# Performance work log

Hardware: AMD Instinct MI355X
Metric: run time of the kernel (lower is better)

Reference implementation:

```python
import math
import jax, jax.numpy as jnp
from jax import lax
import numpy as np

L, B, S, D, H, F = 12, 8, 512, 768, 12, 3072
DH = D // H
REL_POS_BINS, MAX_REL_POS = 32, 128
REL_2D_POS_BINS, MAX_REL_2D_POS = 64, 256
LN_EPS = 1e-12


def _rel_bucket(rel, num_buckets, max_distance):
    # bidirectional relative_position_bucket as in LayoutLMv2
    num_buckets = num_buckets // 2
    ret = (rel > 0).astype(jnp.int32) * num_buckets
    n = jnp.abs(rel)
    max_exact = num_buckets // 2
    is_small = n < max_exact
    n_safe = jnp.maximum(n, 1)  # avoid log(0); masked by is_small anyway
    val_if_large = max_exact + (
        jnp.log(n_safe.astype(jnp.float32) / max_exact)
        / math.log(max_distance / max_exact) * (num_buckets - max_exact)
    ).astype(jnp.int32)
    val_if_large = jnp.minimum(val_if_large, num_buckets - 1)
    return ret + jnp.where(is_small, n.astype(jnp.int32), val_if_large)


def _layernorm(x, g, b):
    mu = jnp.mean(x, axis=-1, keepdims=True)
    var = jnp.var(x, axis=-1, keepdims=True)
    return (x - mu) * lax.rsqrt(var + LN_EPS) * g + b


def _encoder(hidden_states, attention_mask, position_ids, bbox,
             qkv_w, q_bias, v_bias, attn_out_w, attn_out_b, ln1_g, ln1_b,
             inter_w, inter_b, ffn_out_w, ffn_out_b, ln2_g, ln2_b,
             rel_pos_table, rel_x_table, rel_y_table):
    b, s, d = hidden_states.shape
    h = rel_pos_table.shape[1]
    dh = d // h
    # 1D relative position bias: [B,H,S,S]
    rel = position_ids[:, None, :] - position_ids[:, :, None]  # [B,S,S], rel[b,i,j]=p[j]-p[i]
    rp = _rel_bucket(rel, REL_POS_BINS, MAX_REL_POS)
    bias = jnp.transpose(rel_pos_table[rp], (0, 3, 1, 2))
    # 2D spatial bias from bbox x (coord 0) and y (coord 3)
    cx = bbox[:, :, 0]
    cy = bbox[:, :, 3]
    bx = _rel_bucket(cx[:, None, :] - cx[:, :, None], REL_2D_POS_BINS, MAX_REL_2D_POS)
    by = _rel_bucket(cy[:, None, :] - cy[:, :, None], REL_2D_POS_BINS, MAX_REL_2D_POS)
    bias = bias + jnp.transpose(rel_x_table[bx] + rel_y_table[by], (0, 3, 1, 2))
    mask = attention_mask.astype(bool)  # [B,1,1,S], True = masked
    inv_sqrt_dh = 1.0 / math.sqrt(dh)

    def layer(carry, p):
        (qw, qb, vb, aow, aob, g1, b1, iw, ib, fow, fob, g2, b2) = p
        qkv = carry @ qw                      # [B,S,3D] (fast_qkv, no bias)
        q, k, v = jnp.split(qkv, 3, axis=-1)
        q = (q + qb) * inv_sqrt_dh
        v = v + vb
        q = q.reshape(b, s, h, dh)
        k = k.reshape(b, s, h, dh)
        v = v.reshape(b, s, h, dh)
        scores = jnp.einsum('bihd,bjhd->bhij', q, k) + bias
        scores = jnp.where(mask, -jnp.inf, scores.astype(jnp.float32))
        probs = jax.nn.softmax(scores, axis=-1).astype(carry.dtype)
        ctx = jnp.einsum('bhij,bjhd->bihd', probs, v).reshape(b, s, d)
        attn = _layernorm(ctx @ aow + aob + carry, g1, b1)
        ff = jax.nn.gelu(attn @ iw + ib, approximate=False)
        out = _layernorm(ff @ fow + fob + attn, g2, b2)
        return out, None

    params = (qkv_w, q_bias, v_bias, attn_out_w, attn_out_b, ln1_g, ln1_b,
              inter_w, inter_b, ffn_out_w, ffn_out_b, ln2_g, ln2_b)
    out, _ = lax.scan(layer, hidden_states, params)
    return out


def setup_inputs() -> dict:
    key = jax.random.key(0)
    ks = jax.random.split(key, 12)
    w = 0.02
    inp = {
        'hidden_states': jax.random.normal(ks[0], (B, S, D), jnp.float32),
        'attention_mask': jax.random.randint(ks[1], (B, 1, 1, S), 0, 2).astype(jnp.int32),
        'position_ids': jnp.broadcast_to(jnp.arange(S, dtype=jnp.int64), (B, S)),
        'bbox': jax.random.randint(ks[2], (B, S, 4), 0, 1000).astype(jnp.int64),
        'qkv_w': jax.random.normal(ks[3], (L, D, 3 * D), jnp.float32) * w,
        'q_bias': jnp.zeros((L, D), jnp.float32),
        'v_bias': jnp.zeros((L, D), jnp.float32),
        'attn_out_w': jax.random.normal(ks[4], (L, D, D), jnp.float32) * w,
        'attn_out_b': jnp.zeros((L, D), jnp.float32),
        'ln1_g': jnp.ones((L, D), jnp.float32),
        'ln1_b': jnp.zeros((L, D), jnp.float32),
        'inter_w': jax.random.normal(ks[5], (L, D, F), jnp.float32) * w,
        'inter_b': jnp.zeros((L, F), jnp.float32),
        'ffn_out_w': jax.random.normal(ks[6], (L, F, D), jnp.float32) * w,
        'ffn_out_b': jnp.zeros((L, D), jnp.float32),
        'ln2_g': jnp.ones((L, D), jnp.float32),
        'ln2_b': jnp.zeros((L, D), jnp.float32),
        'rel_pos_table': jax.random.normal(ks[7], (REL_POS_BINS, H), jnp.float32) * w,
        'rel_x_table': jax.random.normal(ks[8], (REL_2D_POS_BINS, H), jnp.float32) * w,
        'rel_y_table': jax.random.normal(ks[9], (REL_2D_POS_BINS, H), jnp.float32) * w,
    }
    return inp


def reference(hidden_states, attention_mask, position_ids, bbox,
              qkv_w, q_bias, v_bias, attn_out_w, attn_out_b, ln1_g, ln1_b,
              inter_w, inter_b, ffn_out_w, ffn_out_b, ln2_g, ln2_b,
              rel_pos_table, rel_x_table, rel_y_table):
    return _encoder(hidden_states, attention_mask, position_ids, bbox,
                    qkv_w, q_bias, v_bias, attn_out_w, attn_out_b, ln1_g, ln1_b,
                    inter_w, inter_b, ffn_out_w, ffn_out_b, ln2_g, ln2_b,
                    rel_pos_table, rel_x_table, rel_y_table)
```

## Files before the change

### kernel.cpp

```cpp
#include <hip/hip_runtime.h>
#include <hip/hip_bf16.h>
#include <cstdint>

#define LCONST 12
#define BCONST 8
#define SCONST 512
#define DCONST 768
#define HCONST 12
#define FCONST 3072
#define DH 64

typedef __bf16 bf16x8 __attribute__((ext_vector_type(8)));
typedef float f32x4 __attribute__((ext_vector_type(4)));

__device__ __forceinline__ void gload16(const void* g, void* l) {
    __builtin_amdgcn_global_load_lds(
            (const __attribute__((address_space(1))) void*)g,
            (__attribute__((address_space(3))) void*)l, 16, 0, 0);
}

__device__ __forceinline__ int rbucket(int rel, int nb2, int maxex) {
    int ret = (rel > 0) ? nb2 : 0;
    int n = (rel < 0) ? -rel : rel;
    if (n < maxex) return ret + n;
    const float inv_ln16 = 0.36067376022224085f;
    int v = maxex + (int)(logf((float)n / (float)maxex) * inv_ln16 * (float)(nb2 - maxex));
    if (v > nb2 - 1) v = nb2 - 1;
    return ret + v;
}

__global__ __launch_bounds__(256) void build_idx_kernel(
        const int* __restrict__ pos, const int* __restrict__ bbox,
        int* __restrict__ idx) {
    size_t t = (size_t)blockIdx.x * 256 + threadIdx.x;
    int j = (int)(t & 511);
    int i = (int)((t >> 9) & 511);
    int b = (int)(t >> 18);
    int rp = rbucket(pos[b * SCONST + j] - pos[b * SCONST + i], 16, 8);
    int cxi = bbox[((size_t)b * SCONST + i) * 4 + 0];
    int cxj = bbox[((size_t)b * SCONST + j) * 4 + 0];
    int cyi = bbox[((size_t)b * SCONST + i) * 4 + 3];
    int cyj = bbox[((size_t)b * SCONST + j) * 4 + 3];
    int bx = rbucket(cxj - cxi, 32, 16);
    int by = rbucket(cyj - cyi, 32, 16);
    idx[t] = rp | (bx << 5) | (by << 11);
}

__global__ __launch_bounds__(256) void cvt_kernel(const float* __restrict__ in,
                                                  __bf16* __restrict__ out, int n) {
    int t = blockIdx.x * 256 + threadIdx.x;
    if (t < n) out[t] = (__bf16)in[t];
}

__global__ __launch_bounds__(256) void transpose_cvt_kernel(
        const float* __restrict__ in, __bf16* __restrict__ out, int R, int C) {
    __shared__ float tile[32][33];
    size_t off = (size_t)blockIdx.y * R * C;
    int nct = C >> 5;
    int c0 = (blockIdx.x % nct) << 5;
    int r0 = (blockIdx.x / nct) << 5;
    int tx = threadIdx.x & 31, ty = threadIdx.x >> 5;
#pragma unroll
    for (int i = 0; i < 32; i += 8)
        tile[ty + i][tx] = in[off + (size_t)(r0 + ty + i) * C + c0 + tx];
    __syncthreads();
#pragma unroll
    for (int i = 0; i < 32; i += 8)
        out[off + (size_t)(c0 + ty + i) * R + r0 + tx] = (__bf16)tile[tx][ty + i];
}

template <int MODE>
__global__ __launch_bounds__(256) void gemm_kernel(
        const __bf16* __restrict__ A, const __bf16* __restrict__ Bt,
        int M, int N, int Kc, int ldK,
        const float* __restrict__ cbias, const float* __restrict__ vbias,
        float* __restrict__ part,
        __bf16* __restrict__ outQ, __bf16* __restrict__ outK,
        __bf16* __restrict__ outV, __bf16* __restrict__ outB) {
    __shared__ __align__(16) __bf16 As[128 * 32];
    __shared__ __align__(16) __bf16 Bs[128 * 32];
    int tid = threadIdx.x;
    int wid = tid >> 6, lane = tid & 63, quad = lane >> 4, l16 = lane & 15;
    int nTM = M >> 7;
    int tileM = (blockIdx.x % nTM) << 7;
    int tileN = (blockIdx.x / nTM) << 7;
    int chunk = blockIdx.y;
    int wm = wid >> 1, wn = wid & 1;

    const __bf16* Ab = A + (size_t)chunk * Kc;
    const __bf16* Bb = Bt + (size_t)chunk * Kc;
    const __bf16* gA0 = Ab + (size_t)(tileM + wid * 32 + (lane >> 2)) * ldK + ((lane & 3) << 3);
    const __bf16* gB0 = Bb + (size_t)(tileN + wid * 32 + (lane >> 2)) * ldK + ((lane & 3) << 3);
    __bf16* lA0 = As + wid * 1024;
    __bf16* lB0 = Bs + wid * 1024;

    f32x4 acc[4][4] = {};

    for (int k0 = 0; k0 < Kc; k0 += 32) {
        gload16(gA0 + k0, lA0);
        gload16(gA0 + (size_t)16 * ldK + k0, lA0 + 512);
        gload16(gB0 + k0, lB0);
        gload16(gB0 + (size_t)16 * ldK + k0, lB0 + 512);
        __syncthreads();
        bf16x8 af[4], bfr[4];
#pragma unroll
        for (int mt = 0; mt < 4; mt++)
            af[mt] = *(const bf16x8*)&As[(wm * 64 + mt * 16 + l16) * 32 + quad * 8];
#pragma unroll
        for (int nt = 0; nt < 4; nt++)
            bfr[nt] = *(const bf16x8*)&Bs[(wn * 64 + nt * 16 + l16) * 32 + quad * 8];
#pragma unroll
        for (int mt = 0; mt < 4; mt++)
#pragma unroll
            for (int nt = 0; nt < 4; nt++)
                acc[mt][nt] = __builtin_amdgcn_mfma_f32_16x16x32_bf16(
                        af[mt], bfr[nt], acc[mt][nt], 0, 0, 0);
        __syncthreads();
    }

#pragma unroll
    for (int mt = 0; mt < 4; mt++)
#pragma unroll
        for (int nt = 0; nt < 4; nt++)
#pragma unroll
            for (int r = 0; r < 4; r++) {
                int row = tileM + wm * 64 + mt * 16 + quad * 4 + r;
                int col = tileN + wn * 64 + nt * 16 + l16;
                float v = acc[mt][nt][r];
                if (MODE == 0) {
                    int b = row >> 9, s = row & 511;
                    if (col < 768) {
                        int h = col >> 6, dh = col & 63;
                        float q = (v + cbias[col]) * 0.125f;
                        outQ[(((size_t)b * HCONST + h) * SCONST + s) * DH + dh] = (__bf16)q;
                    } else if (col < 1536) {
                        int c2 = col - 768;
                        int h = c2 >> 6, dh = c2 & 63;
                        outK[(((size_t)b * HCONST + h) * SCONST + s) * DH + dh] = (__bf16)v;
                    } else {
                        int c2 = col - 1536;
                        int h = c2 >> 6, dh = c2 & 63;
                        float vv = v + vbias[c2];
                        outV[(((size_t)b * HCONST + h) * DH + dh) * SCONST + s] = (__bf16)vv;
                    }
                } else if (MODE == 2) {
                    float u = v + cbias[col];
                    float g = 0.5f * u * (1.0f + erff(u * 0.70710678118654752f));
                    outB[(size_t)row * N + col] = (__bf16)g;
                } else {
                    part[(size_t)chunk * M * N + (size_t)row * N + col] = v;
                }
            }
}

__global__ __launch_bounds__(256) void attn_kernel(
        const __bf16* __restrict__ qbuf, const __bf16* __restrict__ kbuf,
        const __bf16* __restrict__ vbuf, const int* __restrict__ idx,
        const int* __restrict__ amask, const float* __restrict__ tpg,
        const float* __restrict__ txg, const float* __restrict__ tyg,
        __bf16* __restrict__ ctx) {
    int bh = blockIdx.x >> 3;
    int i0 = (blockIdx.x & 7) << 6;
    int b = bh / HCONST, h = bh % HCONST;

    __shared__ __align__(16) __bf16 Ks[64 * 64];
    __shared__ __align__(16) __bf16 Vs[64 * 64];
    __shared__ __align__(16) __bf16 Ps[4][16 * 64];
    __shared__ float tp[32], tx[64], ty[64];
    __shared__ float mk[512];

    int tid = threadIdx.x;
    if (tid < 32) tp[tid] = tpg[tid * HCONST + h];
    if (tid < 64) {
        tx[tid] = txg[tid * HCONST + h];
        ty[tid] = tyg[tid * HCONST + h];
    }
    for (int j = tid; j < 512; j += 256)
        mk[j] = amask[b * SCONST + j] ? -INFINITY : 0.0f;

    int wid = tid >> 6, lane = tid & 63, quad = lane >> 4, l16 = lane & 15;

    const __bf16* qrow = qbuf + ((size_t)bh * SCONST + i0 + wid * 16 + l16) * DH;
    bf16x8 qf0 = *(const bf16x8*)(qrow + quad * 8);
    bf16x8 qf1 = *(const bf16x8*)(qrow + 32 + quad * 8);

    const __bf16* kg = kbuf + (size_t)bh * SCONST * DH;
    const __bf16* vg = vbuf + (size_t)bh * DH * SCONST;

    f32x4 O[4] = {};
    float m_r[4] = {-1e30f, -1e30f, -1e30f, -1e30f};
    float l_r[4] = {0.f, 0.f, 0.f, 0.f};

    __syncthreads();

    for (int j0 = 0; j0 < SCONST; j0 += 64) {
        {
            const __bf16* kbase = kg + (size_t)j0 * DH;
#pragma unroll
            for (int s = 0; s < 2; s++) {
                int c = wid * 2 + s;
                gload16(kbase + c * 512 + lane * 8, Ks + c * 512);
                int dh = c * 8 + (lane >> 3), cc = lane & 7;
                gload16(vg + (size_t)dh * SCONST + j0 + cc * 8, Vs + c * 512);
            }
        }
        __syncthreads();

        float sc[4][4];
#pragma unroll
        for (int jt = 0; jt < 4; jt++) {
            f32x4 a = {};
            bf16x8 kf0 = *(const bf16x8*)&Ks[(jt * 16 + l16) * 64 + quad * 8];
            bf16x8 kf1 = *(const bf16x8*)&Ks[(jt * 16 + l16) * 64 + 32 + quad * 8];
            a = __builtin_amdgcn_mfma_f32_16x16x32_bf16(qf0, kf0, a, 0, 0, 0);
            a = __builtin_amdgcn_mfma_f32_16x16x32_bf16(qf1, kf1, a, 0, 0, 0);
#pragma unroll
            for (int r = 0; r < 4; r++) {
                int i = i0 + wid * 16 + quad * 4 + r;
                int j = j0 + jt * 16 + l16;
                int pk = idx[((size_t)b * SCONST + i) * SCONST + j];
                float bias = tp[pk & 31] + tx[(pk >> 5) & 63] + ty[(pk >> 11) & 63];
                sc[jt][r] = a[r] + bias + mk[j];
            }
        }

        float p[4][4];
#pragma unroll
        for (int r = 0; r < 4; r++) {
            float mb = fmaxf(fmaxf(sc[0][r], sc[1][r]), fmaxf(sc[2][r], sc[3][r]));
#pragma unroll
            for (int m = 1; m < 16; m <<= 1) mb = fmaxf(mb, __shfl_xor(mb, m, 64));
            float mn = fmaxf(m_r[r], mb);
            float alpha = __expf(m_r[r] - mn);
            m_r[r] = mn;
            float ls = 0.f;
#pragma unroll
            for (int jt = 0; jt < 4; jt++) {
                float pv = __expf(sc[jt][r] - mn);
                p[jt][r] = pv;
                ls += pv;
            }
#pragma unroll
            for (int m = 1; m < 16; m <<= 1) ls += __shfl_xor(ls, m, 64);
            l_r[r] = l_r[r] * alpha + ls;
#pragma unroll
            for (int nt = 0; nt < 4; nt++) O[nt][r] *= alpha;
        }

        __bf16* pl = &Ps[wid][0];
#pragma unroll
        for (int jt = 0; jt < 4; jt++)
#pragma unroll
            for (int r = 0; r < 4; r++)
                pl[(quad * 4 + r) * 64 + jt * 16 + l16] = (__bf16)p[jt][r];

        bf16x8 pa0 = *(const bf16x8*)&pl[l16 * 64 + quad * 8];
        bf16x8 pa1 = *(const bf16x8*)&pl[l16 * 64 + 32 + quad * 8];
#pragma unroll
        for (int nt = 0; nt < 4; nt++) {
            bf16x8 vb0 = *(const bf16x8*)&Vs[(nt * 16 + l16) * 64 + quad * 8];
            bf16x8 vb1 = *(const bf16x8*)&Vs[(nt * 16 + l16) * 64 + 32 + quad * 8];
            O[nt] = __builtin_amdgcn_mfma_f32_16x16x32_bf16(pa0, vb0, O[nt], 0, 0, 0);
            O[nt] = __builtin_amdgcn_mfma_f32_16x16x32_bf16(pa1, vb1, O[nt], 0, 0, 0);
        }
        __syncthreads();
    }

#pragma unroll
    for (int nt = 0; nt < 4; nt++)
#pragma unroll
        for (int r = 0; r < 4; r++) {
            int i = i0 + wid * 16 + quad * 4 + r;
            int dh = nt * 16 + l16;
            float o = O[nt][r] / l_r[r];
            ctx[((size_t)b * SCONST + i) * DCONST + h * DH + dh] = (__bf16)o;
        }
}

__global__ __launch_bounds__(256) void ln4_kernel(
        const float* __restrict__ part, const float* __restrict__ resid,
        const float* __restrict__ cbias, const float* __restrict__ g,
        const float* __restrict__ bb, float* __restrict__ outF,
        __bf16* __restrict__ outB) {
    const size_t MN = (size_t)4096 * DCONST;
    __shared__ float red[4];
    int row = blockIdx.x, t = threadIdx.x;
    size_t o = (size_t)row * DCONST;
    float v0, v1, v2;
    {
        int c0 = t, c1 = t + 256, c2 = t + 512;
        v0 = part[o + c0] + part[MN + o + c0] + part[2 * MN + o + c0] +
             part[3 * MN + o + c0] + cbias[c0] + resid[o + c0];
        v1 = part[o + c1] + part[MN + o + c1] + part[2 * MN + o + c1] +
             part[3 * MN + o + c1] + cbias[c1] + resid[o + c1];
        v2 = part[o + c2] + part[MN + o + c2] + part[2 * MN + o + c2] +
             part[3 * MN + o + c2] + cbias[c2] + resid[o + c2];
    }
    float s = v0 + v1 + v2;
#pragma unroll
    for (int m = 1; m < 64; m <<= 1) s += __shfl_xor(s, m, 64);
    if ((t & 63) == 0) red[t >> 6] = s;
    __syncthreads();
    s = red[0] + red[1] + red[2] + red[3];
    __syncthreads();
    float mu = s * (1.0f / 768.0f);
    float d0 = v0 - mu, d1 = v1 - mu, d2 = v2 - mu;
    float q = d0 * d0 + d1 * d1 + d2 * d2;
#pragma unroll
    for (int m = 1; m < 64; m <<= 1) q += __shfl_xor(q, m, 64);
    if ((t & 63) == 0) red[t >> 6] = q;
    __syncthreads();
    q = red[0] + red[1] + red[2] + red[3];
    float rstd = rsqrtf(q * (1.0f / 768.0f) + 1e-12f);
    float y0 = d0 * rstd * g[t] + bb[t];
    float y1 = d1 * rstd * g[t + 256] + bb[t + 256];
    float y2 = d2 * rstd * g[t + 512] + bb[t + 512];
    outF[o + t] = y0;
    outF[o + t + 256] = y1;
    outF[o + t + 512] = y2;
    outB[o + t] = (__bf16)y0;
    outB[o + t + 256] = (__bf16)y1;
    outB[o + t + 512] = (__bf16)y2;
}

extern "C" void kernel_launch(void* const* d_in, const int* in_sizes, int n_in,
                              void* d_out, int out_size, void* d_ws, size_t ws_size,
                              hipStream_t stream) {
    const float* hidden = (const float*)d_in[0];
    const int* amask = (const int*)d_in[1];
    const int* pos = (const int*)d_in[2];
    const int* bbox = (const int*)d_in[3];
    const float* qkv_w = (const float*)d_in[4];
    const float* q_bias = (const float*)d_in[5];
    const float* v_bias = (const float*)d_in[6];
    const float* aow = (const float*)d_in[7];
    const float* aob = (const float*)d_in[8];
    const float* ln1g = (const float*)d_in[9];
    const float* ln1b = (const float*)d_in[10];
    const float* iw = (const float*)d_in[11];
    const float* ib = (const float*)d_in[12];
    const float* fow = (const float*)d_in[13];
    const float* fob = (const float*)d_in[14];
    const float* ln2g = (const float*)d_in[15];
    const float* ln2b = (const float*)d_in[16];
    const float* tpt = (const float*)d_in[17];
    const float* txt = (const float*)d_in[18];
    const float* tyt = (const float*)d_in[19];
    float* out = (float*)d_out;

    char* w = (char*)d_ws;
    size_t used = 0;
    auto carve = [&](size_t bytes) {
        char* p = w + used;
        used += (bytes + 255) & ~(size_t)255;
        return p;
    };
    const size_t MT = 4096;
    __bf16* qbuf = (__bf16*)carve(MT * 768 * 2);
    __bf16* kbuf = (__bf16*)carve(MT * 768 * 2);
    __bf16* vbuf = (__bf16*)carve(MT * 768 * 2);
    __bf16* xbf = (__bf16*)carve(MT * 768 * 2);
    __bf16* ctxbf = (__bf16*)carve(MT * 768 * 2);
    float* attnf = (float*)carve(MT * 768 * 4);
    __bf16* attnbf = (__bf16*)carve(MT * 768 * 2);
    __bf16* ffbf = (__bf16*)carve(MT * 3072 * 2);
    float* part = (float*)carve(4 * MT * 768 * 4);
    int* idxb = (int*)carve((size_t)BCONST * SCONST * SCONST * 4);

    const size_t wq_sz = (size_t)2304 * 768 * 2;
    const size_t wa_sz = (size_t)768 * 768 * 2;
    const size_t wi_sz = (size_t)3072 * 768 * 2;
    const size_t wf_sz = (size_t)768 * 3072 * 2;
    const size_t wsum = wq_sz + wa_sz + wi_sz + wf_sz;
    bool full = (ws_size >= used + 12 * wsum + (12 * 4 + 4) * 256);
    int nlw = full ? 12 : 1;
    __bf16* wqT = (__bf16*)carve(wq_sz * nlw);
    __bf16* waT = (__bf16*)carve(wa_sz * nlw);
    __bf16* wiT = (__bf16*)carve(wi_sz * nlw);
    __bf16* wfT = (__bf16*)carve(wf_sz * nlw);

    build_idx_kernel<<<(BCONST * SCONST * SCONST) / 256, 256, 0, stream>>>(pos, bbox, idxb);
    cvt_kernel<<<(int)(MT * 768 / 256), 256, 0, stream>>>(hidden, xbf, (int)(MT * 768));

    if (full) {
        transpose_cvt_kernel<<<dim3((2304 / 32) * (768 / 32), 12), 256, 0, stream>>>(
                qkv_w, wqT, 768, 2304);
        transpose_cvt_kernel<<<dim3((768 / 32) * (768 / 32), 12), 256, 0, stream>>>(
                aow, waT, 768, 768);
        transpose_cvt_kernel<<<dim3((3072 / 32) * (768 / 32), 12), 256, 0, stream>>>(
                iw, wiT, 768, 3072);
        transpose_cvt_kernel<<<dim3((768 / 32) * (3072 / 32), 12), 256, 0, stream>>>(
                fow, wfT, 3072, 768);
    }

    for (int l = 0; l < LCONST; l++) {
        __bf16* wq_l = wqT + (full ? (size_t)l * 2304 * 768 : 0);
        __bf16* wa_l = waT + (full ? (size_t)l * 768 * 768 : 0);
        __bf16* wi_l = wiT + (full ? (size_t)l * 3072 * 768 : 0);
        __bf16* wf_l = wfT + (full ? (size_t)l * 768 * 3072 : 0);
        if (!full) {
            transpose_cvt_kernel<<<dim3((2304 / 32) * (768 / 32), 1), 256, 0, stream>>>(
                    qkv_w + (size_t)l * 768 * 2304, wq_l, 768, 2304);
            transpose_cvt_kernel<<<dim3((768 / 32) * (768 / 32), 1), 256, 0, stream>>>(
                    aow + (size_t)l * 768 * 768, wa_l, 768, 768);
            transpose_cvt_kernel<<<dim3((3072 / 32) * (768 / 32), 1), 256, 0, stream>>>(
                    iw + (size_t)l * 768 * 3072, wi_l, 768, 3072);
            transpose_cvt_kernel<<<dim3((768 / 32) * (3072 / 32), 1), 256, 0, stream>>>(
                    fow + (size_t)l * 3072 * 768, wf_l, 3072, 768);
        }

        gemm_kernel<0><<<dim3((4096 / 128) * (2304 / 128), 1), 256, 0, stream>>>(
                xbf, wq_l, 4096, 2304, 768, 768, q_bias + (size_t)l * 768,
                v_bias + (size_t)l * 768, nullptr, qbuf, kbuf, vbuf, nullptr);

        attn_kernel<<<BCONST * HCONST * (SCONST / 64), 256, 0, stream>>>(
                qbuf, kbuf, vbuf, idxb, amask, tpt, txt, tyt, ctxbf);

        gemm_kernel<4><<<dim3((4096 / 128) * (768 / 128), 4), 256, 0, stream>>>(
                ctxbf, wa_l, 4096, 768, 192, 768, nullptr, nullptr, part,
                nullptr, nullptr, nullptr, nullptr);
        const float* xres = (l == 0) ? hidden : out;
        ln4_kernel<<<4096, 256, 0, stream>>>(part, xres, aob + (size_t)l * 768,
                                             ln1g + (size_t)l * 768,
                                             ln1b + (size_t)l * 768, attnf, attnbf);

        gemm_kernel<2><<<dim3((4096 / 128) * (3072 / 128), 1), 256, 0, stream>>>(
                attnbf, wi_l, 4096, 3072, 768, 768, ib + (size_t)l * 3072, nullptr,
                nullptr, nullptr, nullptr, nullptr, ffbf);

        gemm_kernel<4><<<dim3((4096 / 128) * (768 / 128), 4), 256, 0, stream>>>(
                ffbf, wf_l, 4096, 768, 768, 3072, nullptr, nullptr, part,
                nullptr, nullptr, nullptr, nullptr);
        ln4_kernel<<<4096, 256, 0, stream>>>(part, attnf, fob + (size_t)l * 768,
                                             ln2g + (size_t)l * 768,
                                             ln2b + (size_t)l * 768, out, xbf);
    }
}
```

Before: 2.887 ms.

## Precompute per-head bf16 attention bias and deepen GEMM K-step to 64

Replaces the packed bucket-index buffer with a precomputed bf16 bias tensor [B,H,S,S] that already includes the three table lookups and the padding mask. The attention kernel streams each bias tile into LDS with async global-to-LDS loads instead of doing per-element index loads and shared-table gathers. This trades scattered gathers for a larger, contiguous read each layer (bf16, so about half the bytes per element of the int index buffer, but once per head). The GEMM now loads two 32-wide K slices per barrier pair, halving the number of syncs, at the cost of double the LDS per block. Rounding the bias and mask to bf16 adds a small accuracy risk.

```diff
diff --git a/kernel.cpp b/kernel.cpp
--- a/kernel.cpp
+++ b/kernel.cpp
@@ -29,21 +29,33 @@
     return ret + v;
 }
 
-__global__ __launch_bounds__(256) void build_idx_kernel(
+__global__ __launch_bounds__(256) void bias_kernel(
         const int* __restrict__ pos, const int* __restrict__ bbox,
-        int* __restrict__ idx) {
-    size_t t = (size_t)blockIdx.x * 256 + threadIdx.x;
-    int j = (int)(t & 511);
-    int i = (int)((t >> 9) & 511);
-    int b = (int)(t >> 18);
-    int rp = rbucket(pos[b * SCONST + j] - pos[b * SCONST + i], 16, 8);
+        const int* __restrict__ amask, const float* __restrict__ tpt,
+        const float* __restrict__ txt, const float* __restrict__ tyt,
+        __bf16* __restrict__ biasM) {
+    __shared__ float tpl[32 * 12], txl[64 * 12], tyl[64 * 12];
+    int t = threadIdx.x;
+    for (int k = t; k < 32 * 12; k += 256) tpl[k] = tpt[k];
+    for (int k = t; k < 64 * 12; k += 256) { txl[k] = txt[k]; tyl[k] = tyt[k]; }
+    int b = blockIdx.x >> 9, i = blockIdx.x & 511;
+    int pi = pos[b * SCONST + i];
     int cxi = bbox[((size_t)b * SCONST + i) * 4 + 0];
-    int cxj = bbox[((size_t)b * SCONST + j) * 4 + 0];
     int cyi = bbox[((size_t)b * SCONST + i) * 4 + 3];
-    int cyj = bbox[((size_t)b * SCONST + j) * 4 + 3];
-    int bx = rbucket(cxj - cxi, 32, 16);
-    int by = rbucket(cyj - cyi, 32, 16);
-    idx[t] = rp | (bx << 5) | (by << 11);
+    __syncthreads();
+#pragma unroll
+    for (int s = 0; s < 2; s++) {
+        int j = t + s * 256;
+        int rp = rbucket(pos[b * SCONST + j] - pi, 16, 8);
+        int bx = rbucket(bbox[((size_t)b * SCONST + j) * 4 + 0] - cxi, 32, 16);
+        int by = rbucket(bbox[((size_t)b * SCONST + j) * 4 + 3] - cyi, 32, 16);
+        float mk = amask[b * SCONST + j] ? -INFINITY : 0.0f;
+#pragma unroll
+        for (int h = 0; h < 12; h++) {
+            float v = tpl[rp * 12 + h] + txl[bx * 12 + h] + tyl[by * 12 + h] + mk;
+            biasM[(((size_t)(b * HCONST + h)) * SCONST + i) * SCONST + j] = (__bf16)v;
+        }
+    }
 }
 
 __global__ __launch_bounds__(256) void cvt_kernel(const float* __restrict__ in,
@@ -77,8 +89,8 @@
         float* __restrict__ part,
         __bf16* __restrict__ outQ, __bf16* __restrict__ outK,
         __bf16* __restrict__ outV, __bf16* __restrict__ outB) {
-    __shared__ __align__(16) __bf16 As[128 * 32];
-    __shared__ __align__(16) __bf16 Bs[128 * 32];
+    __shared__ __align__(16) __bf16 As[2][128 * 32];
+    __shared__ __align__(16) __bf16 Bs[2][128 * 32];
     int tid = threadIdx.x;
     int wid = tid >> 6, lane = tid & 63, quad = lane >> 4, l16 = lane & 15;
     int nTM = M >> 7;
@@ -91,30 +103,34 @@
     const __bf16* Bb = Bt + (size_t)chunk * Kc;
     const __bf16* gA0 = Ab + (size_t)(tileM + wid * 32 + (lane >> 2)) * ldK + ((lane & 3) << 3);
     const __bf16* gB0 = Bb + (size_t)(tileN + wid * 32 + (lane >> 2)) * ldK + ((lane & 3) << 3);
-    __bf16* lA0 = As + wid * 1024;
-    __bf16* lB0 = Bs + wid * 1024;
 
     f32x4 acc[4][4] = {};
 
-    for (int k0 = 0; k0 < Kc; k0 += 32) {
-        gload16(gA0 + k0, lA0);
-        gload16(gA0 + (size_t)16 * ldK + k0, lA0 + 512);
-        gload16(gB0 + k0, lB0);
-        gload16(gB0 + (size_t)16 * ldK + k0, lB0 + 512);
+    for (int k0 = 0; k0 < Kc; k0 += 64) {
+#pragma unroll
+        for (int p = 0; p < 2; p++) {
+            gload16(gA0 + k0 + p * 32, &As[p][wid * 1024]);
+            gload16(gA0 + (size_t)16 * ldK + k0 + p * 32, &As[p][wid * 1024 + 512]);
+            gload16(gB0 + k0 + p * 32, &Bs[p][wid * 1024]);
+            gload16(gB0 + (size_t)16 * ldK + k0 + p * 32, &Bs[p][wid * 1024 + 512]);
+        }
         __syncthreads();
-        bf16x8 af[4], bfr[4];
-#pragma unroll
-        for (int mt = 0; mt < 4; mt++)
-            af[mt] = *(const bf16x8*)&As[(wm * 64 + mt * 16 + l16) * 32 + quad * 8];
-#pragma unroll
-        for (int nt = 0; nt < 4; nt++)
-            bfr[nt] = *(const bf16x8*)&Bs[(wn * 64 + nt * 16 + l16) * 32 + quad * 8];
-#pragma unroll
-        for (int mt = 0; mt < 4; mt++)
+#pragma unroll
+        for (int p = 0; p < 2; p++) {
+            bf16x8 af[4], bfr[4];
+#pragma unroll
+            for (int mt = 0; mt < 4; mt++)
+                af[mt] = *(const bf16x8*)&As[p][(wm * 64 + mt * 16 + l16) * 32 + quad * 8];
 #pragma unroll
             for (int nt = 0; nt < 4; nt++)
-                acc[mt][nt] = __builtin_amdgcn_mfma_f32_16x16x32_bf16(
-                        af[mt], bfr[nt], acc[mt][nt], 0, 0, 0);
+                bfr[nt] = *(const bf16x8*)&Bs[p][(wn * 64 + nt * 16 + l16) * 32 + quad * 8];
+#pragma unroll
+            for (int mt = 0; mt < 4; mt++)
+#pragma unroll
+                for (int nt = 0; nt < 4; nt++)
+                    acc[mt][nt] = __builtin_amdgcn_mfma_f32_16x16x32_bf16(
+                            af[mt], bfr[nt], acc[mt][nt], 0, 0, 0);
+        }
         __syncthreads();
     }
 
@@ -155,29 +171,18 @@
 
 __global__ __launch_bounds__(256) void attn_kernel(
         const __bf16* __restrict__ qbuf, const __bf16* __restrict__ kbuf,
-        const __bf16* __restrict__ vbuf, const int* __restrict__ idx,
-        const int* __restrict__ amask, const float* __restrict__ tpg,
-        const float* __restrict__ txg, const float* __restrict__ tyg,
+        const __bf16* __restrict__ vbuf, const __bf16* __restrict__ biasM,
         __bf16* __restrict__ ctx) {
     int bh = blockIdx.x >> 3;
     int i0 = (blockIdx.x & 7) << 6;
-    int b = bh / HCONST, h = bh % HCONST;
+    int b = bh / HCONST;
 
     __shared__ __align__(16) __bf16 Ks[64 * 64];
     __shared__ __align__(16) __bf16 Vs[64 * 64];
+    __shared__ __align__(16) __bf16 Bi[64 * 64];
     __shared__ __align__(16) __bf16 Ps[4][16 * 64];
-    __shared__ float tp[32], tx[64], ty[64];
-    __shared__ float mk[512];
 
     int tid = threadIdx.x;
-    if (tid < 32) tp[tid] = tpg[tid * HCONST + h];
-    if (tid < 64) {
-        tx[tid] = txg[tid * HCONST + h];
-        ty[tid] = tyg[tid * HCONST + h];
-    }
-    for (int j = tid; j < 512; j += 256)
-        mk[j] = amask[b * SCONST + j] ? -INFINITY : 0.0f;
-
     int wid = tid >> 6, lane = tid & 63, quad = lane >> 4, l16 = lane & 15;
 
     const __bf16* qrow = qbuf + ((size_t)bh * SCONST + i0 + wid * 16 + l16) * DH;
@@ -186,12 +191,11 @@
 
     const __bf16* kg = kbuf + (size_t)bh * SCONST * DH;
     const __bf16* vg = vbuf + (size_t)bh * DH * SCONST;
+    const __bf16* bg = biasM + (size_t)bh * SCONST * SCONST;
 
     f32x4 O[4] = {};
     float m_r[4] = {-1e30f, -1e30f, -1e30f, -1e30f};
     float l_r[4] = {0.f, 0.f, 0.f, 0.f};
-
-    __syncthreads();
 
     for (int j0 = 0; j0 < SCONST; j0 += 64) {
         {
@@ -202,6 +206,8 @@
                 gload16(kbase + c * 512 + lane * 8, Ks + c * 512);
                 int dh = c * 8 + (lane >> 3), cc = lane & 7;
                 gload16(vg + (size_t)dh * SCONST + j0 + cc * 8, Vs + c * 512);
+                gload16(bg + (size_t)(i0 + c * 8 + (lane >> 3)) * SCONST + j0 + cc * 8,
+                        Bi + c * 512);
             }
         }
         __syncthreads();
@@ -216,11 +222,8 @@
             a = __builtin_amdgcn_mfma_f32_16x16x32_bf16(qf1, kf1, a, 0, 0, 0);
 #pragma unroll
             for (int r = 0; r < 4; r++) {
-                int i = i0 + wid * 16 + quad * 4 + r;
-                int j = j0 + jt * 16 + l16;
-                int pk = idx[((size_t)b * SCONST + i) * SCONST + j];
-                float bias = tp[pk & 31] + tx[(pk >> 5) & 63] + ty[(pk >> 11) & 63];
-                sc[jt][r] = a[r] + bias + mk[j];
+                float bias = (float)Bi[(wid * 16 + quad * 4 + r) * 64 + jt * 16 + l16];
+                sc[jt][r] = a[r] + bias;
             }
         }
 
@@ -273,7 +276,7 @@
             int i = i0 + wid * 16 + quad * 4 + r;
             int dh = nt * 16 + l16;
             float o = O[nt][r] / l_r[r];
-            ctx[((size_t)b * SCONST + i) * DCONST + h * DH + dh] = (__bf16)o;
+            ctx[((size_t)b * SCONST + i) * DCONST + (bh % HCONST) * DH + dh] = (__bf16)o;
         }
 }
 
@@ -365,7 +368,7 @@
     __bf16* attnbf = (__bf16*)carve(MT * 768 * 2);
     __bf16* ffbf = (__bf16*)carve(MT * 3072 * 2);
     float* part = (float*)carve(4 * MT * 768 * 4);
-    int* idxb = (int*)carve((size_t)BCONST * SCONST * SCONST * 4);
+    __bf16* biasM = (__bf16*)carve((size_t)BCONST * HCONST * SCONST * SCONST * 2);
 
     const size_t wq_sz = (size_t)2304 * 768 * 2;
     const size_t wa_sz = (size_t)768 * 768 * 2;
@@ -379,7 +382,8 @@
     __bf16* wiT = (__bf16*)carve(wi_sz * nlw);
     __bf16* wfT = (__bf16*)carve(wf_sz * nlw);
 
-    build_idx_kernel<<<(BCONST * SCONST * SCONST) / 256, 256, 0, stream>>>(pos, bbox, idxb);
+    bias_kernel<<<BCONST * SCONST, 256, 0, stream>>>(pos, bbox, amask, tpt, txt, tyt,
+                                                     biasM);
     cvt_kernel<<<(int)(MT * 768 / 256), 256, 0, stream>>>(hidden, xbf, (int)(MT * 768));
 
     if (full) {
@@ -414,7 +418,7 @@
                 v_bias + (size_t)l * 768, nullptr, qbuf, kbuf, vbuf, nullptr);
 
         attn_kernel<<<BCONST * HCONST * (SCONST / 64), 256, 0, stream>>>(
-                qbuf, kbuf, vbuf, idxb, amask, tpt, txt, tyt, ctxbf);
+                qbuf, kbuf, vbuf, biasM, ctxbf);
 
         gemm_kernel<4><<<dim3((4096 / 128) * (768 / 128), 4), 256, 0, stream>>>(
                 ctxbf, wa_l, 4096, 768, 192, 768, nullptr, nullptr, part,
```

New measurement: 2.976 ms. +3.1%, slower.
